# Optimization experiments

Measured on AMD Instinct MI355X. Metric: run time of the kernel, lower is better.

Reference implementation:

```python
import jax, jax.numpy as jnp
import numpy as np

T, MEM, B, DM, N, D = 1024, 1024, 4, 1024, 16, 64
C = MEM + T
SCALE = 1.0 / D ** 0.5
LN_EPS = 1e-5


def _rel_shift(x):
    # x: [T, C, B, N] -> Transformer-XL relative shift
    t, c = x.shape[0], x.shape[1]
    zero_pad = jnp.zeros((t, 1) + x.shape[2:], x.dtype)
    x_padded = jnp.concatenate([zero_pad, x], axis=1)  # [T, C+1, B, N]
    x_padded = x_padded.reshape((c + 1, t) + x.shape[2:])
    return x_padded[1:].reshape(x.shape)


def setup_inputs() -> dict:
    key = jax.random.key(0)
    ks = jax.random.split(key, 8)
    h = jax.random.normal(ks[0], (T, B, DM), jnp.float32)
    m = jax.random.normal(ks[1], (MEM, B, DM), jnp.float32)
    r = jax.random.normal(ks[2], (C, DM), jnp.float32)
    # causal mask with memory: query i (global pos MEM+i) may attend to j <= MEM+i
    mask = (jnp.arange(C)[None, :] > (jnp.arange(T)[:, None] + MEM))[:, :, None]  # [T,C,1] bool, True=disallow
    W_qkv = jax.random.normal(ks[3], (DM, 3 * N * D), jnp.float32) * 0.02
    W_r = jax.random.normal(ks[4], (DM, N * D), jnp.float32) * 0.02
    W_o = jax.random.normal(ks[5], (N * D, DM), jnp.float32) * 0.02
    r_w_bias = jax.random.normal(ks[6], (N, D), jnp.float32)
    r_r_bias = jax.random.normal(ks[7], (N, D), jnp.float32)
    ln_gamma = jnp.ones((DM,), jnp.float32)
    ln_beta = jnp.zeros((DM,), jnp.float32)
    return {"h": h, "m": m, "r": r, "mask": mask, "W_qkv": W_qkv, "W_r": W_r,
            "W_o": W_o, "r_w_bias": r_w_bias, "r_r_bias": r_r_bias,
            "ln_gamma": ln_gamma, "ln_beta": ln_beta}


def reference(h, m, r, mask, W_qkv, W_r, W_o, r_w_bias, r_r_bias, ln_gamma, ln_beta):
    t, b = h.shape[0], h.shape[1]
    c = r.shape[0]
    cat = jnp.concatenate([m, h], axis=0)          # [C, B, DM]
    w_heads = cat @ W_qkv                           # [C, B, 3*N*D]
    w_q, w_k, w_v = jnp.split(w_heads, 3, axis=-1)
    w_q = w_q[-t:].reshape(t, b, N, D)              # [T,B,N,D]
    w_k = w_k.reshape(c, b, N, D)                   # [C,B,N,D]
    w_v = w_v.reshape(c, b, N, D)                   # [C,B,N,D]
    r_k = (r @ W_r).reshape(c, N, D)                # [C,N,D]
    AC = jnp.einsum('ibnd,jbnd->ijbn', w_q + r_w_bias, w_k)
    BD = jnp.einsum('ibnd,jnd->ijbn', w_q + r_r_bias, r_k)
    BD = _rel_shift(BD)
    score = (AC + BD) * SCALE                       # [T,C,B,N]
    score = jnp.where(mask[:, :, :, None], jnp.float32(-65000.0), score.astype(jnp.float32)).astype(score.dtype)
    prob = jax.nn.softmax(score, axis=1)
    vec = jnp.einsum('ijbn,jbnd->ibnd', prob, w_v).reshape(t, b, N * D)
    attn_out = vec @ W_o                            # [T,B,DM]
    x = h + attn_out
    mu = jnp.mean(x, axis=-1, keepdims=True)
    var = jnp.mean((x - mu) ** 2, axis=-1, keepdims=True)
    return (x - mu) * jax.lax.rsqrt(var + LN_EPS) * ln_gamma + ln_beta
```

## Files before the change

### kernel.cpp

```cpp
#include <hip/hip_runtime.h>
#include <stdint.h>

#define T_LEN 1024
#define MEM_LEN 1024
#define C_LEN 2048
#define B_SZ 4
#define DM_ 1024
#define NH 16
#define HD 64

typedef __attribute__((ext_vector_type(8))) short short8;
typedef __attribute__((ext_vector_type(4))) float f32x4;
typedef __attribute__((ext_vector_type(4))) unsigned short ushort4v;
typedef __attribute__((ext_vector_type(4))) float float4v;

__device__ __forceinline__ unsigned short f2bf(float f) {
  union { float f; unsigned int u; } v; v.f = f;
  unsigned int r = v.u + 0x7fffu + ((v.u >> 16) & 1u);
  return (unsigned short)(r >> 16);
}
__device__ __forceinline__ float bf2f(unsigned short b) {
  union { unsigned int u; float f; } v; v.u = ((unsigned int)b) << 16;
  return v.f;
}
__device__ __forceinline__ unsigned int cvtpk(float lo, float hi) {
  unsigned int r;
  asm("v_cvt_pk_bf16_f32 %0, %1, %2" : "=v"(r) : "v"(lo), "v"(hi));
  return r;
}
__device__ __forceinline__ f32x4 mfma16(short8 a, short8 b, f32x4 c) {
  return __builtin_amdgcn_mfma_f32_16x16x32_bf16(a, b, c, 0, 0, 0);
}

__global__ void k_cat_convert(const float* __restrict__ m, const float* __restrict__ h,
                              unsigned short* __restrict__ outB) {
  int idx = blockIdx.x * 256 + threadIdx.x;
  const int MQ = (MEM_LEN * B_SZ * DM_) / 4;
  float4v v;
  if (idx < MQ) v = ((const float4v*)m)[idx];
  else          v = ((const float4v*)h)[idx - MQ];
  ushort4v o;
  o.x = f2bf(v.x); o.y = f2bf(v.y); o.z = f2bf(v.z); o.w = f2bf(v.w);
  ((ushort4v*)outB)[idx] = o;
}

__global__ void k_f32_to_bf16(const float* __restrict__ in, unsigned short* __restrict__ outB, int nq) {
  int idx = blockIdx.x * 256 + threadIdx.x;
  if (idx >= nq) return;
  float4v v = ((const float4v*)in)[idx];
  ushort4v o;
  o.x = f2bf(v.x); o.y = f2bf(v.y); o.z = f2bf(v.z); o.w = f2bf(v.w);
  ((ushort4v*)outB)[idx] = o;
}

__global__ void k_transpose_bf16(const float* __restrict__ in, unsigned short* __restrict__ out,
                                 int R, int Ccols) {
  __shared__ float tile[32][33];
  int c0 = blockIdx.x * 32, r0 = blockIdx.y * 32;
  int tx = threadIdx.x & 31, ty = threadIdx.x >> 5;
#pragma unroll
  for (int p = 0; p < 4; ++p)
    tile[ty + 8 * p][tx] = in[(size_t)(r0 + ty + 8 * p) * Ccols + c0 + tx];
  __syncthreads();
#pragma unroll
  for (int p = 0; p < 4; ++p)
    out[(size_t)(c0 + ty + 8 * p) * R + r0 + tx] = f2bf(tile[tx][ty + 8 * p]);
}

template <int MODE>
__global__ __launch_bounds__(256) void k_gemm(const unsigned short* __restrict__ A,
                                              const unsigned short* __restrict__ BT,
                                              void* __restrict__ out1, void* __restrict__ out2,
                                              int M, int N, int K, int ldc) {
  __shared__ unsigned short As[128 * 64];
  __shared__ unsigned short Bs[128 * 64];
  const int tid = threadIdx.x;
  const int w = tid >> 6, l = tid & 63;
  const int wm = w >> 1, wn = w & 1;
  const int lg = l >> 4, lr = l & 15;
  const int gx = gridDim.x;
  const int pid = blockIdx.y * gx + blockIdx.x;
  const int xcd = pid & 7;
  const int idx = pid >> 3;
  const int cb = idx % gx;
  const int rb = (idx / gx) * 8 + xcd;
  const int m0 = rb * 128, n0 = cb * 128;
  f32x4 acc[4][4] = {};
  const int lrow8 = l >> 3;
  const int scol = (l & 7) * 8;
  const unsigned short* Abase = A + (size_t)m0 * K;
  const unsigned short* Bbase = BT + (size_t)n0 * K;
  for (int kt = 0; kt < K; kt += 64) {
    __syncthreads();
#pragma unroll
    for (int q = 0; q < 4; ++q) {
      int chunk = w * 4 + q;
      int row = chunk * 8 + lrow8;
      __builtin_amdgcn_global_load_lds(
          (const __attribute__((address_space(1))) void*)(Abase + (size_t)row * K + kt + scol),
          (__attribute__((address_space(3))) void*)(As + chunk * 512), 16, 0, 0);
      __builtin_amdgcn_global_load_lds(
          (const __attribute__((address_space(1))) void*)(Bbase + (size_t)row * K + kt + scol),
          (__attribute__((address_space(3))) void*)(Bs + chunk * 512), 16, 0, 0);
    }
    __syncthreads();
#pragma unroll
    for (int ks = 0; ks < 2; ++ks) {
      short8 a[4], bb[4];
#pragma unroll
      for (int mi = 0; mi < 4; ++mi)
        a[mi] = *(const short8*)&As[(wm * 64 + mi * 16 + lr) * 64 + ks * 32 + lg * 8];
#pragma unroll
      for (int ni = 0; ni < 4; ++ni)
        bb[ni] = *(const short8*)&Bs[(wn * 64 + ni * 16 + lr) * 64 + ks * 32 + lg * 8];
#pragma unroll
      for (int mi = 0; mi < 4; ++mi)
#pragma unroll
        for (int ni = 0; ni < 4; ++ni)
          acc[mi][ni] = mfma16(a[mi], bb[ni], acc[mi][ni]);
    }
  }
#pragma unroll
  for (int mi = 0; mi < 4; ++mi)
#pragma unroll
    for (int ni = 0; ni < 4; ++ni)
#pragma unroll
      for (int r = 0; r < 4; ++r) {
        int row = m0 + wm * 64 + mi * 16 + lg * 4 + r;
        int cc = n0 + wn * 64 + ni * 16 + lr;
        float val = acc[mi][ni][r];
        if (MODE == 1) {
          ((float*)out1)[(size_t)row * ldc + cc] = val;
        } else if (MODE == 2) {
          int nn = (cc & 1023) >> 6, d = cc & 63;
          int c = row >> 2, b = row & 3;
          size_t addr = ((size_t)((b * 16 + nn) * 2048 + c)) * 64 + d;
          unsigned short* dst = (cc < 1024) ? (unsigned short*)out1 : (unsigned short*)out2;
          dst[addr] = f2bf(val);
        } else if (MODE == 3) {
          int nn = cc >> 6, d = cc & 63;
          int t = row >> 2, b = row & 3;
          ((unsigned short*)out1)[((size_t)((b * 16 + nn) * 1024 + t)) * 64 + d] = f2bf(val);
        } else {
          int nn = cc >> 6, d = cc & 63;
          ((unsigned short*)out1)[((size_t)(nn * 2048 + row)) * 64 + d] = f2bf(val);
        }
      }
}

__global__ void k_vt(const unsigned short* __restrict__ Vp, unsigned short* __restrict__ VT) {
  __shared__ unsigned short tile[64][72];
  int c0 = blockIdx.x * 64;
  int n = blockIdx.y, b = blockIdx.z;
  int t = threadIdx.x;
  const unsigned short* src = Vp + ((size_t)((b * 16 + n) * 2048 + c0)) * 64;
#pragma unroll
  for (int p = 0; p < 16; ++p) {
    int idx = p * 256 + t;
    int r = idx >> 6, d = idx & 63;
    tile[d][r] = src[(size_t)r * 64 + d];
  }
  __syncthreads();
#pragma unroll
  for (int p = 0; p < 16; ++p) {
    int idx = p * 256 + t;
    int d = idx >> 6, c = idx & 63;
    VT[(size_t)((b * 16 + n) * 64 + d) * 2048 + c0 + c] = tile[d][c];
  }
}

__device__ __forceinline__ void stage_tile(const unsigned short* __restrict__ Kbase,
                                           const unsigned short* __restrict__ Vbase,
                                           unsigned short* ksBuf, unsigned short* vsBuf,
                                           int j0, int tid) {
#pragma unroll
  for (int q = 0; q < 2; ++q) {
    int chunk = q * 256 + tid;
    int row = chunk >> 3;
    int slot = chunk & 7;
    int ss = slot ^ (row & 7);
    __builtin_amdgcn_global_load_lds(
        (const __attribute__((address_space(1))) void*)(Kbase + (size_t)(j0 + row) * 64 + ss * 8),
        (__attribute__((address_space(3))) void*)(ksBuf + chunk * 8), 16, 0, 0);
    __builtin_amdgcn_global_load_lds(
        (const __attribute__((address_space(1))) void*)(Vbase + (size_t)row * 2048 + j0 + ss * 8),
        (__attribute__((address_space(3))) void*)(vsBuf + chunk * 8), 16, 0, 0);
  }
}

__global__ __launch_bounds__(256) void k_attn(const unsigned short* __restrict__ Qp,
                                              const unsigned short* __restrict__ Kp,
                                              const unsigned short* __restrict__ VT,
                                              const unsigned short* __restrict__ Rkp,
                                              const float* __restrict__ rwb,
                                              const float* __restrict__ rrb,
                                              unsigned short* __restrict__ po,
                                              float* __restrict__ psumG) {
  __shared__ __align__(16) unsigned short Ks[2][64 * 64];
  __shared__ __align__(16) unsigned short Vs[2][64 * 64];
  __shared__ unsigned short P[4][16][72];
  const int tid = threadIdx.x;
  const int w = tid >> 6, l = tid & 63;
  const int lg = l >> 4, lr = l & 15;
  const int L = blockIdx.x;
  const int bnlo = L & 7;
  const int rest = L >> 3;
  const int bnhi = rest / 48;
  const int inner = rest - bnhi * 48;
  const int xt = inner / 3;
  const int s  = inner - xt * 3;
  const int bn = bnhi * 8 + bnlo;
  const int i0 = xt * 64;
  const int n = bn & 15, b = bn >> 4;
  const int wrow = i0 + w * 16;

  const int ntile = xt + 17;
  const int t0 = (s * ntile) / 3;
  const int t1 = ((s + 1) * ntile) / 3;

  const unsigned short* Kbase = Kp + (size_t)bn * 2048 * 64;
  const unsigned short* Vbase = VT + (size_t)bn * 64 * 2048;
  const unsigned short* Rkbase = Rkp + (size_t)n * 2048 * 64;

  short8 aq0u, aq1u, aq0v, aq1v;
  {
    const unsigned short* qp = Qp + (size_t)(bn * 1024 + wrow + lr) * 64 + lg * 8;
    short8 q0 = *(const short8*)qp;
    short8 q1 = *(const short8*)(qp + 32);
    const float* up = rwb + n * 64 + lg * 8;
    const float* vp = rrb + n * 64 + lg * 8;
#pragma unroll
    for (int e = 0; e < 8; ++e) {
      float q0f = bf2f((unsigned short)q0[e]);
      float q1f = bf2f((unsigned short)q1[e]);
      aq0u[e] = (short)f2bf(q0f + up[e]);
      aq1u[e] = (short)f2bf(q1f + up[e + 32]);
      aq0v[e] = (short)f2bf(q0f + vp[e]);
      aq1v[e] = (short)f2bf(q1f + vp[e + 32]);
    }
  }
  float psum[4];
  f32x4 o[4];
#pragma unroll
  for (int r = 0; r < 4; ++r) psum[r] = 0.f;
#pragma unroll
  for (int df = 0; df < 4; ++df) o[df] = (f32x4){0.f, 0.f, 0.f, 0.f};

  stage_tile(Kbase, Vbase, Ks[0], Vs[0], t0 * 64, tid);
  stage_tile(Kbase, Vbase, Ks[1], Vs[1], (t0 + 1) * 64, tid);

  const float EXPC = 0.18033688011112042f;

  for (int jt = t0; jt < t1; ++jt) {
    const int j0 = jt * 64;
    const int cur = (jt - t0) & 1;
    if (jt + 1 < t1) { asm volatile("s_waitcnt vmcnt(4)" ::: "memory"); }
    else             { asm volatile("s_waitcnt vmcnt(0)" ::: "memory"); }
    __builtin_amdgcn_s_barrier();

    f32x4 sac[4];
#pragma unroll
    for (int jf = 0; jf < 4; ++jf) sac[jf] = (f32x4){0.f, 0.f, 0.f, 0.f};
#pragma unroll
    for (int jf = 0; jf < 4; ++jf) {
      int row = jf * 16 + lr;
      int rx = row & 7;
      short8 k0 = *(const short8*)&Ks[cur][row * 64 + ((lg ^ rx) * 8)];
      short8 k1 = *(const short8*)&Ks[cur][row * 64 + (((4 + lg) ^ rx) * 8)];
      sac[jf] = mfma16(aq0u, k0, sac[jf]);
      sac[jf] = mfma16(aq1u, k1, sac[jf]);
    }
    const int kbw = j0 + 1008 - i0 - w * 16;
    f32x4 gb[5];
#pragma unroll
    for (int jg = 0; jg < 5; ++jg) {
      int rowK = kbw + jg * 16 + lr;
      short8 b0 = {}, b1 = {};
      if (rowK < C_LEN) {
        const unsigned short* rp = Rkbase + (size_t)rowK * 64 + lg * 8;
        b0 = *(const short8*)rp;
        b1 = *(const short8*)(rp + 32);
      }
      f32x4 g = (f32x4){0.f, 0.f, 0.f, 0.f};
      g = mfma16(aq0v, b0, g);
      g = mfma16(aq1v, b1, g);
      gb[jg] = g;
    }
    const bool needMask = (j0 + 63 > i0 + w * 16 + MEM_LEN);
    float p[4][4];
#pragma unroll
    for (int r = 0; r < 4; ++r) {
      const int R = lg * 4 + r;
      const int delta = lr + 15 - R;
      const int src = (l & 48) | (delta & 15);
      float v0 = __shfl(gb[0][r], src);
      float v1 = __shfl(gb[1][r], src);
      float v2 = __shfl(gb[2][r], src);
      float v3 = __shfl(gb[3][r], src);
      float v4 = __shfl(gb[4][r], src);
      const bool hi = delta >= 16;
      float bd0 = hi ? v1 : v0;
      float bd1 = hi ? v2 : v1;
      float bd2 = hi ? v3 : v2;
      float bd3 = hi ? v4 : v3;
      float e0 = exp2f((sac[0][r] + bd0) * EXPC);
      float e1 = exp2f((sac[1][r] + bd1) * EXPC);
      float e2 = exp2f((sac[2][r] + bd2) * EXPC);
      float e3 = exp2f((sac[3][r] + bd3) * EXPC);
      if (needMask) {
        const int jlim = i0 + w * 16 + R + MEM_LEN;
        int j = j0 + lr;
        e0 = (j > jlim) ? 0.f : e0;  j += 16;
        e1 = (j > jlim) ? 0.f : e1;  j += 16;
        e2 = (j > jlim) ? 0.f : e2;  j += 16;
        e3 = (j > jlim) ? 0.f : e3;
      }
      p[0][r] = e0; p[1][r] = e1; p[2][r] = e2; p[3][r] = e3;
    }
#pragma unroll
    for (int jf = 0; jf < 4; ++jf)
#pragma unroll
      for (int r = 0; r < 4; ++r) psum[r] += p[jf][r];
#pragma unroll
    for (int r = 0; r < 4; ++r) {
      unsigned int a01 = cvtpk(p[0][r], p[1][r]);
      unsigned int a23 = cvtpk(p[2][r], p[3][r]);
      const int R = lg * 4 + r;
      P[w][R][lr]      = (unsigned short)a01;
      P[w][R][16 + lr] = (unsigned short)(a01 >> 16);
      P[w][R][32 + lr] = (unsigned short)a23;
      P[w][R][48 + lr] = (unsigned short)(a23 >> 16);
    }
#pragma unroll
    for (int ks = 0; ks < 2; ++ks) {
      short8 ap = *(const short8*)&P[w][lr][ks * 32 + lg * 8];
#pragma unroll
      for (int df = 0; df < 4; ++df) {
        int row = df * 16 + lr;
        int rx = row & 7;
        short8 vv = *(const short8*)&Vs[cur][row * 64 + (((ks * 4 + lg) ^ rx) * 8)];
        o[df] = mfma16(ap, vv, o[df]);
      }
    }
    __builtin_amdgcn_s_barrier();
    if (jt + 2 < t1)
      stage_tile(Kbase, Vbase, Ks[cur], Vs[cur], (jt + 2) * 64, tid);
  }
  const int pbase = (bn * 16 + xt) * 3 + s;
  unsigned short* poB = po + (size_t)pbase * 4096;
#pragma unroll
  for (int r = 0; r < 4; ++r) {
    float v = psum[r];
    v += __shfl_xor(v, 1);
    v += __shfl_xor(v, 2);
    v += __shfl_xor(v, 4);
    v += __shfl_xor(v, 8);
    if (lr == 0) psumG[pbase * 64 + w * 16 + lg * 4 + r] = v;
  }
#pragma unroll
  for (int df = 0; df < 4; ++df)
#pragma unroll
    for (int r = 0; r < 4; ++r)
      poB[(w * 16 + lg * 4 + r) * 64 + df * 16 + lr] = f2bf(o[df][r]);
}

__global__ __launch_bounds__(256) void k_ared(const unsigned short* __restrict__ po,
                                              const float* __restrict__ psumG,
                                              unsigned short* __restrict__ vec) {
  const int idx = blockIdx.x;
  const int tid = threadIdx.x;
  const int bn = idx >> 4, xt = idx & 15;
  const int b = bn >> 4, n = bn & 15;
  __shared__ float rs[64];
  if (tid < 64) {
    const float* q = psumG + idx * 192;
    rs[tid] = q[tid] + q[tid + 64] + q[tid + 128];
  }
  __syncthreads();
  const ushort4v* p0 = (const ushort4v*)(po + (size_t)(idx * 3 + 0) * 4096);
  const ushort4v* p1 = (const ushort4v*)(po + (size_t)(idx * 3 + 1) * 4096);
  const ushort4v* p2 = (const ushort4v*)(po + (size_t)(idx * 3 + 2) * 4096);
#pragma unroll
  for (int k = 0; k < 4; ++k) {
    int e = tid + k * 256;
    int row = e >> 4, d4 = e & 15;
    ushort4v a = p0[e], bb = p1[e], c = p2[e];
    float inv = 1.f / rs[row];
    int t = xt * 64 + row;
    ushort4v ov;
    ov.x = f2bf((bf2f(a.x) + bf2f(bb.x) + bf2f(c.x)) * inv);
    ov.y = f2bf((bf2f(a.y) + bf2f(bb.y) + bf2f(c.y)) * inv);
    ov.z = f2bf((bf2f(a.z) + bf2f(bb.z) + bf2f(c.z)) * inv);
    ov.w = f2bf((bf2f(a.w) + bf2f(bb.w) + bf2f(c.w)) * inv);
    *(ushort4v*)&vec[(size_t)(t * 4 + b) * 1024 + n * 64 + d4 * 4] = ov;
  }
}

__global__ __launch_bounds__(256) void k_ln(const float* __restrict__ xg, const float* __restrict__ h,
                                            const float* __restrict__ gamma, const float* __restrict__ beta,
                                            float* __restrict__ out) {
  const int row = blockIdx.x;
  const int t = threadIdx.x;
  __shared__ float red1[4], red2[4];
  float4v xv = ((const float4v*)(xg + (size_t)row * 1024))[t];
  float4v hv = ((const float4v*)(h + (size_t)row * 1024))[t];
  float x0 = xv.x + hv.x, x1 = xv.y + hv.y, x2 = xv.z + hv.z, x3 = xv.w + hv.w;
  float s = x0 + x1 + x2 + x3;
#pragma unroll
  for (int off = 1; off < 64; off <<= 1) s += __shfl_xor(s, off);
  if ((t & 63) == 0) red1[t >> 6] = s;
  __syncthreads();
  float mean = (red1[0] + red1[1] + red1[2] + red1[3]) * (1.f / 1024.f);
  float d0 = x0 - mean, d1 = x1 - mean, d2 = x2 - mean, d3 = x3 - mean;
  float q = d0 * d0 + d1 * d1 + d2 * d2 + d3 * d3;
#pragma unroll
  for (int off = 1; off < 64; off <<= 1) q += __shfl_xor(q, off);
  if ((t & 63) == 0) red2[t >> 6] = q;
  __syncthreads();
  float var = (red2[0] + red2[1] + red2[2] + red2[3]) * (1.f / 1024.f);
  float rs = rsqrtf(var + 1e-5f);
  float4v gv = ((const float4v*)gamma)[t];
  float4v bv = ((const float4v*)beta)[t];
  float4v ov;
  ov.x = d0 * rs * gv.x + bv.x;
  ov.y = d1 * rs * gv.y + bv.y;
  ov.z = d2 * rs * gv.z + bv.z;
  ov.w = d3 * rs * gv.w + bv.w;
  ((float4v*)(out + (size_t)row * 1024))[t] = ov;
}

extern "C" void kernel_launch(void* const* d_in, const int* in_sizes, int n_in,
                              void* d_out, int out_size, void* d_ws, size_t ws_size,
                              hipStream_t stream) {
  (void)in_sizes; (void)n_in; (void)out_size; (void)ws_size;
  const float* h    = (const float*)d_in[0];
  const float* m    = (const float*)d_in[1];
  const float* r    = (const float*)d_in[2];
  const float* Wqkv = (const float*)d_in[4];
  const float* Wr   = (const float*)d_in[5];
  const float* Wo   = (const float*)d_in[6];
  const float* rwb  = (const float*)d_in[7];
  const float* rrb  = (const float*)d_in[8];
  const float* gam  = (const float*)d_in[9];
  const float* bet  = (const float*)d_in[10];
  float* out = (float*)d_out;

  char* ws = (char*)d_ws;
  unsigned short* catB   = (unsigned short*)(ws + 0);
  unsigned short* WqkvT  = (unsigned short*)(ws + 16777216);
  unsigned short* WrT    = (unsigned short*)(ws + 23068672);
  unsigned short* WoT    = (unsigned short*)(ws + 25165824);
  unsigned short* Vp     = (unsigned short*)(ws + 27262976);
  unsigned short* po     = (unsigned short*)(ws + 44040192);
  unsigned short* VT     = (unsigned short*)(ws + 81788928);
  unsigned short* vec    = (unsigned short*)(ws + 99221504);
  float* xbuf            = (float*)(ws + 107610112);
  unsigned short* rB     = (unsigned short*)(ws + 124387328);
  unsigned short* Kp     = (unsigned short*)(ws + 128581632);
  unsigned short* Qp     = (unsigned short*)(ws + 145358848);
  unsigned short* Rkp    = (unsigned short*)(ws + 153747456);
  float* psumG = (float*)(ws + 124387328);

  hipLaunchKernelGGL(k_cat_convert, dim3(8192), dim3(256), 0, stream, m, h, catB);
  hipLaunchKernelGGL(k_f32_to_bf16, dim3(2048), dim3(256), 0, stream, r, rB, 524288);
  hipLaunchKernelGGL(k_transpose_bf16, dim3(96, 32), dim3(256), 0, stream, Wqkv, WqkvT, 1024, 3072);
  hipLaunchKernelGGL(k_transpose_bf16, dim3(32, 32), dim3(256), 0, stream, Wr, WrT, 1024, 1024);
  hipLaunchKernelGGL(k_transpose_bf16, dim3(32, 32), dim3(256), 0, stream, Wo, WoT, 1024, 1024);
  hipLaunchKernelGGL(k_gemm<2>, dim3(16, 64), dim3(256), 0, stream,
                     catB, WqkvT + (size_t)1024 * 1024, (void*)Kp, (void*)Vp, 8192, 2048, 1024, 0);
  hipLaunchKernelGGL(k_gemm<3>, dim3(8, 32), dim3(256), 0, stream,
                     catB + (size_t)4096 * 1024, WqkvT, (void*)Qp, nullptr, 4096, 1024, 1024, 0);
  hipLaunchKernelGGL(k_gemm<4>, dim3(8, 16), dim3(256), 0, stream,
                     rB, WrT, (void*)Rkp, nullptr, 2048, 1024, 1024, 0);
  hipLaunchKernelGGL(k_vt, dim3(32, 16, 4), dim3(256), 0, stream, Vp, VT);
  hipLaunchKernelGGL(k_attn, dim3(3072), dim3(256), 0, stream, Qp, Kp, VT, Rkp, rwb, rrb, po, psumG);
  hipLaunchKernelGGL(k_ared, dim3(1024), dim3(256), 0, stream, po, psumG, vec);
  hipLaunchKernelGGL(k_gemm<1>, dim3(8, 32), dim3(256), 0, stream,
                     vec, WoT, (void*)xbuf, nullptr, 4096, 1024, 1024, 1024);
  hipLaunchKernelGGL(k_ln, dim3(4096), dim3(256), 0, stream, xbuf, h, gam, bet, out);
}
```

Before: 328.0 us.

## Merge conversion and transpose launches, add MFMA priority hints, widen reduce loads

Folds the cat and r bf16 conversions into one kernel and the three weight transposes into a single z-indexed launch, which cuts kernel launch count and tail overhead. Wraps the QK and PV MFMA loops in the attention kernel with s_setprio to favour matrix issue across waves. Widens the partial-output reduction to 8-element vector loads and stores. The transpose grid now includes early-exit blocks for the narrower matrices.

```diff
diff --git a/kernel.cpp b/kernel.cpp
--- a/kernel.cpp
+++ b/kernel.cpp
@@ -12,6 +12,7 @@
 typedef __attribute__((ext_vector_type(8))) short short8;
 typedef __attribute__((ext_vector_type(4))) float f32x4;
 typedef __attribute__((ext_vector_type(4))) unsigned short ushort4v;
+typedef __attribute__((ext_vector_type(8))) unsigned short ushort8v;
 typedef __attribute__((ext_vector_type(4))) float float4v;
 
 __device__ __forceinline__ unsigned short f2bf(float f) {
@@ -32,30 +33,34 @@
   return __builtin_amdgcn_mfma_f32_16x16x32_bf16(a, b, c, 0, 0, 0);
 }
 
-__global__ void k_cat_convert(const float* __restrict__ m, const float* __restrict__ h,
-                              unsigned short* __restrict__ outB) {
+__global__ void k_convert_all(const float* __restrict__ m, const float* __restrict__ h,
+                              const float* __restrict__ r,
+                              unsigned short* __restrict__ catB,
+                              unsigned short* __restrict__ rB) {
   int idx = blockIdx.x * 256 + threadIdx.x;
   const int MQ = (MEM_LEN * B_SZ * DM_) / 4;
+  const int CQ = 2 * MQ;
   float4v v;
-  if (idx < MQ) v = ((const float4v*)m)[idx];
-  else          v = ((const float4v*)h)[idx - MQ];
+  unsigned short* dst;
+  int di;
+  if (idx < MQ)      { v = ((const float4v*)m)[idx];       dst = catB; di = idx; }
+  else if (idx < CQ) { v = ((const float4v*)h)[idx - MQ];  dst = catB; di = idx; }
+  else               { v = ((const float4v*)r)[idx - CQ];  dst = rB;   di = idx - CQ; }
   ushort4v o;
   o.x = f2bf(v.x); o.y = f2bf(v.y); o.z = f2bf(v.z); o.w = f2bf(v.w);
-  ((ushort4v*)outB)[idx] = o;
-}
-
-__global__ void k_f32_to_bf16(const float* __restrict__ in, unsigned short* __restrict__ outB, int nq) {
-  int idx = blockIdx.x * 256 + threadIdx.x;
-  if (idx >= nq) return;
-  float4v v = ((const float4v*)in)[idx];
-  ushort4v o;
-  o.x = f2bf(v.x); o.y = f2bf(v.y); o.z = f2bf(v.z); o.w = f2bf(v.w);
-  ((ushort4v*)outB)[idx] = o;
-}
-
-__global__ void k_transpose_bf16(const float* __restrict__ in, unsigned short* __restrict__ out,
-                                 int R, int Ccols) {
+  ((ushort4v*)dst)[di] = o;
+}
+
+__global__ void k_transpose_w(const float* __restrict__ Wqkv, const float* __restrict__ Wr,
+                              const float* __restrict__ Wo,
+                              unsigned short* __restrict__ WqkvT, unsigned short* __restrict__ WrT,
+                              unsigned short* __restrict__ WoT) {
   __shared__ float tile[32][33];
+  const int z = blockIdx.z;
+  const int Ccols = (z == 0) ? 3072 : 1024;
+  if (blockIdx.x * 32 >= Ccols) return;
+  const float* in = (z == 0) ? Wqkv : (z == 1) ? Wr : Wo;
+  unsigned short* out = (z == 0) ? WqkvT : (z == 1) ? WrT : WoT;
   int c0 = blockIdx.x * 32, r0 = blockIdx.y * 32;
   int tx = threadIdx.x & 31, ty = threadIdx.x >> 5;
 #pragma unroll
@@ -64,7 +69,7 @@
   __syncthreads();
 #pragma unroll
   for (int p = 0; p < 4; ++p)
-    out[(size_t)(c0 + ty + 8 * p) * R + r0 + tx] = f2bf(tile[tx][ty + 8 * p]);
+    out[(size_t)(c0 + ty + 8 * p) * 1024 + r0 + tx] = f2bf(tile[tx][ty + 8 * p]);
 }
 
 template <int MODE>
@@ -261,6 +266,7 @@
     f32x4 sac[4];
 #pragma unroll
     for (int jf = 0; jf < 4; ++jf) sac[jf] = (f32x4){0.f, 0.f, 0.f, 0.f};
+    __builtin_amdgcn_s_setprio(1);
 #pragma unroll
     for (int jf = 0; jf < 4; ++jf) {
       int row = jf * 16 + lr;
@@ -270,6 +276,7 @@
       sac[jf] = mfma16(aq0u, k0, sac[jf]);
       sac[jf] = mfma16(aq1u, k1, sac[jf]);
     }
+    __builtin_amdgcn_s_setprio(0);
     const int kbw = j0 + 1008 - i0 - w * 16;
     f32x4 gb[5];
 #pragma unroll
@@ -331,6 +338,7 @@
       P[w][R][32 + lr] = (unsigned short)a23;
       P[w][R][48 + lr] = (unsigned short)(a23 >> 16);
     }
+    __builtin_amdgcn_s_setprio(1);
 #pragma unroll
     for (int ks = 0; ks < 2; ++ks) {
       short8 ap = *(const short8*)&P[w][lr][ks * 32 + lg * 8];
@@ -342,6 +350,7 @@
         o[df] = mfma16(ap, vv, o[df]);
       }
     }
+    __builtin_amdgcn_s_setprio(0);
     __builtin_amdgcn_s_barrier();
     if (jt + 2 < t1)
       stage_tile(Kbase, Vbase, Ks[cur], Vs[cur], (jt + 2) * 64, tid);
@@ -377,22 +386,21 @@
     rs[tid] = q[tid] + q[tid + 64] + q[tid + 128];
   }
   __syncthreads();
-  const ushort4v* p0 = (const ushort4v*)(po + (size_t)(idx * 3 + 0) * 4096);
-  const ushort4v* p1 = (const ushort4v*)(po + (size_t)(idx * 3 + 1) * 4096);
-  const ushort4v* p2 = (const ushort4v*)(po + (size_t)(idx * 3 + 2) * 4096);
-#pragma unroll
-  for (int k = 0; k < 4; ++k) {
+  const ushort8v* p0 = (const ushort8v*)(po + (size_t)(idx * 3 + 0) * 4096);
+  const ushort8v* p1 = (const ushort8v*)(po + (size_t)(idx * 3 + 1) * 4096);
+  const ushort8v* p2 = (const ushort8v*)(po + (size_t)(idx * 3 + 2) * 4096);
+#pragma unroll
+  for (int k = 0; k < 2; ++k) {
     int e = tid + k * 256;
-    int row = e >> 4, d4 = e & 15;
-    ushort4v a = p0[e], bb = p1[e], c = p2[e];
+    int row = e >> 3, d8 = e & 7;
+    ushort8v a = p0[e], bb = p1[e], c = p2[e];
     float inv = 1.f / rs[row];
     int t = xt * 64 + row;
-    ushort4v ov;
-    ov.x = f2bf((bf2f(a.x) + bf2f(bb.x) + bf2f(c.x)) * inv);
-    ov.y = f2bf((bf2f(a.y) + bf2f(bb.y) + bf2f(c.y)) * inv);
-    ov.z = f2bf((bf2f(a.z) + bf2f(bb.z) + bf2f(c.z)) * inv);
-    ov.w = f2bf((bf2f(a.w) + bf2f(bb.w) + bf2f(c.w)) * inv);
-    *(ushort4v*)&vec[(size_t)(t * 4 + b) * 1024 + n * 64 + d4 * 4] = ov;
+    ushort8v ov;
+#pragma unroll
+    for (int q = 0; q < 8; ++q)
+      ov[q] = f2bf((bf2f(a[q]) + bf2f(bb[q]) + bf2f(c[q])) * inv);
+    *(ushort8v*)&vec[(size_t)(t * 4 + b) * 1024 + n * 64 + d8 * 8] = ov;
   }
 }
 
@@ -461,11 +469,9 @@
   unsigned short* Rkp    = (unsigned short*)(ws + 153747456);
   float* psumG = (float*)(ws + 124387328);
 
-  hipLaunchKernelGGL(k_cat_convert, dim3(8192), dim3(256), 0, stream, m, h, catB);
-  hipLaunchKernelGGL(k_f32_to_bf16, dim3(2048), dim3(256), 0, stream, r, rB, 524288);
-  hipLaunchKernelGGL(k_transpose_bf16, dim3(96, 32), dim3(256), 0, stream, Wqkv, WqkvT, 1024, 3072);
-  hipLaunchKernelGGL(k_transpose_bf16, dim3(32, 32), dim3(256), 0, stream, Wr, WrT, 1024, 1024);
-  hipLaunchKernelGGL(k_transpose_bf16, dim3(32, 32), dim3(256), 0, stream, Wo, WoT, 1024, 1024);
+  hipLaunchKernelGGL(k_convert_all, dim3(10240), dim3(256), 0, stream, m, h, r, catB, rB);
+  hipLaunchKernelGGL(k_transpose_w, dim3(96, 32, 3), dim3(256), 0, stream,
+                     Wqkv, Wr, Wo, WqkvT, WrT, WoT);
   hipLaunchKernelGGL(k_gemm<2>, dim3(16, 64), dim3(256), 0, stream,
                      catB, WqkvT + (size_t)1024 * 1024, (void*)Kp, (void*)Vp, 8192, 2048, 1024, 0);
   hipLaunchKernelGGL(k_gemm<3>, dim3(8, 32), dim3(256), 0, stream,
```

Measured after the change: 322.9 us. Within noise of the previous version (-1.5%).
